# Performance work log

Measured on AMD Instinct MI355X. Metric: run time of the kernel, lower is better.

## Reference

```python
import jax, jax.numpy as jnp
import numpy as np

B, N, S = 2, 16384, 4096
IN_CH, OUT_CH = 256, 128

def setup_inputs() -> dict:
    key = jax.random.key(0)
    ks = jax.random.split(key, 8)
    down_xyzp = jax.random.normal(ks[0], (B, S, 4), dtype=jnp.float32)
    down_features = jax.random.normal(ks[1], (B, S, IN_CH), dtype=jnp.float32)
    ori_xyzp = jax.random.normal(ks[2], (B, N, 4), dtype=jnp.float32)
    ori_features = jax.random.normal(ks[3], (B, N, OUT_CH), dtype=jnp.float32)
    # Linear params (torch nn.Linear: y = x @ W.T + b); store as [in,out] for einsum
    W1 = jax.random.normal(ks[4], (IN_CH, OUT_CH), dtype=jnp.float32) / np.sqrt(IN_CH)
    b1 = jnp.zeros((OUT_CH,), dtype=jnp.float32)
    W2 = jax.random.normal(ks[5], (OUT_CH, OUT_CH), dtype=jnp.float32) / np.sqrt(OUT_CH)
    b2 = jnp.zeros((OUT_CH,), dtype=jnp.float32)
    return {"down_xyzp": down_xyzp, "down_features": down_features,
            "ori_xyzp": ori_xyzp, "ori_features": ori_features,
            "W1": W1, "b1": b1, "W2": W2, "b2": b2}

def reference(down_xyzp, down_features, ori_xyzp, ori_features, W1, b1, W2, b2):
    down_f = down_features @ W1 + b1          # [B,S,OUT]
    ori_f = ori_features @ W2 + b2            # [B,N,OUT]
    ori_xyz = ori_xyzp[..., :3]               # [B,N,3]
    down_xyz = down_xyzp[..., :3]             # [B,S,3]
    # squared pairwise dists [B,N,S] via expansion (avoids [B,N,S,3] intermediate)
    d2 = (jnp.sum(ori_xyz**2, -1)[:, :, None]
          + jnp.sum(down_xyz**2, -1)[:, None, :]
          - 2.0 * jnp.einsum('bnd,bsd->bns', ori_xyz, down_xyz))
    neg_top, idx = jax.lax.top_k(-d2, 3)      # 3 smallest dists, ascending
    dists = -neg_top                          # [B,N,3]
    dist_recip = 1.0 / (dists + 1e-8)
    weight = dist_recip / jnp.sum(dist_recip, axis=2, keepdims=True)  # [B,N,3]
    gathered = jax.vmap(lambda f, i: f[i])(down_f, idx)               # [B,N,3,OUT]
    interpolated = jnp.sum(gathered * weight[..., None], axis=2)      # [B,N,OUT]
    return ori_f + interpolated
```

## Files before the change

kernel.cpp:

```cpp
#include <hip/hip_runtime.h>
#include <hip/hip_bf16.h>
#include <float.h>

constexpr int B   = 2;
constexpr int N   = 16384;
constexpr int S   = 4096;
constexpr int INC = 256;
constexpr int OUTC = 128;

typedef short short4_t __attribute__((ext_vector_type(4)));
typedef short short8_t __attribute__((ext_vector_type(8)));
typedef float f32x4    __attribute__((ext_vector_type(4)));

__device__ __forceinline__ unsigned short f2bf(float f) {
    unsigned u = __builtin_bit_cast(unsigned, f);
    u += 0x7fffu + ((u >> 16) & 1u);
    return (unsigned short)(u >> 16);
}

template <int K, int ROWS>
__global__ __launch_bounds__(256) void k_mfma(const float* __restrict__ f,
                                              const float* __restrict__ W,
                                              const float* __restrict__ bias,
                                              float* __restrict__ outf) {
    constexpr int MF = ROWS / 16;
    constexpr int KS = K / 32;
    __shared__ __align__(16) short smem[K * 128];

    const int tid  = threadIdx.x;
    const int lane = tid & 63;
    const int wv   = tid >> 6;
    const int rowbase = blockIdx.x * ROWS;
    const int lo16 = lane & 15;
    const int hi8  = (lane >> 4) * 8;

    const float4* w4 = reinterpret_cast<const float4*>(W);
    for (int n = tid; n < K * 32; n += 256) {
        const float4 u = w4[n];
        short4_t s = { (short)f2bf(u.x), (short)f2bf(u.y),
                       (short)f2bf(u.z), (short)f2bf(u.w) };
        *reinterpret_cast<short4_t*>(&smem[n * 4]) = s;
    }
    __syncthreads();

    short8_t bf[KS][2];
    #pragma unroll
    for (int ks = 0; ks < KS; ++ks) {
        #pragma unroll
        for (int c = 0; c < 2; ++c) {
            const int col = wv * 32 + c * 16 + lo16;
            #pragma unroll
            for (int r = 0; r < 8; ++r)
                bf[ks][c][r] = smem[(ks * 32 + hi8 + r) * 128 + col];
        }
    }
    __syncthreads();

    const float4* a4 = reinterpret_cast<const float4*>(f + (size_t)rowbase * K);
    for (int n = tid; n < ROWS * K / 8; n += 256) {
        const int row   = n / (K / 8);
        const int k8    = (n % (K / 8)) * 8;
        const int base4 = (row * K + k8) >> 2;
        const float4 u = a4[base4];
        const float4 v = a4[base4 + 1];
        short8_t s = { (short)f2bf(u.x), (short)f2bf(u.y), (short)f2bf(u.z), (short)f2bf(u.w),
                       (short)f2bf(v.x), (short)f2bf(v.y), (short)f2bf(v.z), (short)f2bf(v.w) };
        const int idx = (row * K + k8) ^ ((row & 7) << 3);
        *reinterpret_cast<short8_t*>(&smem[idx]) = s;
    }
    __syncthreads();

    f32x4 acc[MF][2];
    #pragma unroll
    for (int m = 0; m < MF; ++m) {
        #pragma unroll
        for (int c = 0; c < 2; ++c) acc[m][c] = (f32x4){0.f, 0.f, 0.f, 0.f};
    }

    const int axor = (lane & 7) << 3;
    #pragma unroll
    for (int ks = 0; ks < KS; ++ks) {
        #pragma unroll
        for (int m = 0; m < MF; ++m) {
            const int aidx = ((m * 16 + lo16) * K + ks * 32 + hi8) ^ axor;
            const short8_t af = *reinterpret_cast<const short8_t*>(&smem[aidx]);
            acc[m][0] = __builtin_amdgcn_mfma_f32_16x16x32_bf16(af, bf[ks][0], acc[m][0], 0, 0, 0);
            acc[m][1] = __builtin_amdgcn_mfma_f32_16x16x32_bf16(af, bf[ks][1], acc[m][1], 0, 0, 0);
        }
    }

    #pragma unroll
    for (int c = 0; c < 2; ++c) {
        const int col = wv * 32 + c * 16 + lo16;
        const float bb = bias[col];
        #pragma unroll
        for (int m = 0; m < MF; ++m) {
            #pragma unroll
            for (int r = 0; r < 4; ++r) {
                const int row = rowbase + m * 16 + (lane >> 4) * 4 + r;
                outf[(size_t)row * 128 + col] = acc[m][c][r] + bb;
            }
        }
    }
}

#define INS3M(d0, d1, d2, i0, i1, i2, dd, ss)                               \
    {                                                                       \
        const bool c0 = (dd) < d0, c1 = (dd) < d1, c2 = (dd) < d2;          \
        i2 = c1 ? i1 : (c2 ? (ss) : i2);                                    \
        i1 = c0 ? i0 : (c1 ? (ss) : i1);                                    \
        i0 = c0 ? (ss) : i0;                                                \
        d2 = fminf(fmaxf((dd), d1), d2);                                    \
        d1 = fminf(fmaxf((dd), d0), d1);                                    \
        d0 = fminf(d0, (dd));                                               \
    }

#define INS3L(d0, d1, d2, i0, i1, i2, dd, ss)                               \
    {                                                                       \
        const bool c0 = ((dd) < d0) | (((dd) == d0) & ((ss) < i0));         \
        const bool c1 = ((dd) < d1) | (((dd) == d1) & ((ss) < i1));         \
        const bool c2 = ((dd) < d2) | (((dd) == d2) & ((ss) < i2));         \
        i2 = c1 ? i1 : (c2 ? (ss) : i2);                                    \
        i1 = c0 ? i0 : (c1 ? (ss) : i1);                                    \
        i0 = c0 ? (ss) : i0;                                                \
        d2 = c1 ? d1 : (c2 ? (dd) : d2);                                    \
        d1 = c0 ? d0 : (c1 ? (dd) : d1);                                    \
        d0 = c0 ? (dd) : d0;                                                \
    }

__global__ __launch_bounds__(256) void k_interp(const float4* __restrict__ dxyzp,
                                                const float4* __restrict__ oxyzp,
                                                const float*  __restrict__ downf,
                                                float*        __restrict__ out) {
    __shared__ float4 sx[16 * 65];
    __shared__ int    si[16 * 3];
    __shared__ float  sw[16 * 3];

    const int b     = blockIdx.x >> 10;
    const int qbase = (blockIdx.x & 1023) * 16;

    const int lane = threadIdx.x & 63;
    const int wave = threadIdx.x >> 6;
    const int sp   = lane & 15;
    const int qs   = lane >> 4;
    const int slot = wave * 4 + qs;

    const float4 o = oxyzp[(size_t)b * N + qbase + slot];
    const float sumo = __fadd_rn(__fadd_rn(__fmul_rn(o.x, o.x), __fmul_rn(o.y, o.y)),
                                 __fmul_rn(o.z, o.z));

    float a0 = FLT_MAX, a1 = FLT_MAX, a2 = FLT_MAX;
    int   ai0 = 0, ai1 = 0, ai2 = 0;

    const float4* dpb = dxyzp + (size_t)b * S;

    for (int c = 0; c < 4; ++c) {
        if (c > 0) __syncthreads();

        const float4* dpc = dpb + c * 1024;
        for (int j = threadIdx.x; j < 1024; j += 256) {
            float4 v = dpc[j];
            const float ss = __fadd_rn(__fadd_rn(__fmul_rn(v.x, v.x), __fmul_rn(v.y, v.y)),
                                       __fmul_rn(v.z, v.z));
            float4 w;
            w.x = v.x + v.x;
            w.y = v.y + v.y;
            w.z = v.z + v.z;
            w.w = ss;
            sx[(j >> 6) * 65 + (j & 63)] = w;
        }
        __syncthreads();

        const float4* base = &sx[sp * 65];
        const int g0 = c * 1024 + sp * 64;

        #pragma unroll 4
        for (int i = 0; i < 64; ++i) {
            const float4 q = base[i];
            const float dot2 = __fadd_rn(__fadd_rn(__fmul_rn(q.x, o.x), __fmul_rn(q.y, o.y)),
                                         __fmul_rn(q.z, o.z));
            const float dd = __fsub_rn(__fadd_rn(sumo, q.w), dot2);
            INS3M(a0, a1, a2, ai0, ai1, ai2, dd, g0 + i);
        }
    }

    #pragma unroll
    for (int m = 1; m <= 8; m <<= 1) {
        const float nd0 = __shfl_xor(a0, m, 64);
        const float nd1 = __shfl_xor(a1, m, 64);
        const float nd2 = __shfl_xor(a2, m, 64);
        const int   ni0 = __shfl_xor(ai0, m, 64);
        const int   ni1 = __shfl_xor(ai1, m, 64);
        const int   ni2 = __shfl_xor(ai2, m, 64);
        INS3L(a0, a1, a2, ai0, ai1, ai2, nd0, ni0);
        INS3L(a0, a1, a2, ai0, ai1, ai2, nd1, ni1);
        INS3L(a0, a1, a2, ai0, ai1, ai2, nd2, ni2);
    }

    if (sp == 0) {
        const float r0 = 1.0f / (a0 + 1e-8f);
        const float r1 = 1.0f / (a1 + 1e-8f);
        const float r2 = 1.0f / (a2 + 1e-8f);
        const float rs = __fadd_rn(__fadd_rn(r0, r1), r2);
        si[slot * 3 + 0] = ai0;
        si[slot * 3 + 1] = ai1;
        si[slot * 3 + 2] = ai2;
        sw[slot * 3 + 0] = r0 / rs;
        sw[slot * 3 + 1] = r1 / rs;
        sw[slot * 3 + 2] = r2 / rs;
    }
    __syncthreads();

    const int ch = threadIdx.x & 127;
    const int hf = threadIdx.x >> 7;
    const float* df = downf + (size_t)b * S * OUTC;
    float* ob = out + ((size_t)b * N + qbase) * OUTC;

    for (int pp = hf; pp < 16; pp += 2) {
        const int   j0 = si[pp * 3 + 0];
        const int   j1 = si[pp * 3 + 1];
        const int   j2 = si[pp * 3 + 2];
        const float w0 = sw[pp * 3 + 0];
        const float w1 = sw[pp * 3 + 1];
        const float w2 = sw[pp * 3 + 2];
        const float g = __fadd_rn(
            __fadd_rn(__fmul_rn(w0, df[(size_t)j0 * OUTC + ch]),
                      __fmul_rn(w1, df[(size_t)j1 * OUTC + ch])),
            __fmul_rn(w2, df[(size_t)j2 * OUTC + ch]));
        ob[(size_t)pp * OUTC + ch] += g;
    }
}


extern "C" void kernel_launch(void* const* d_in, const int* in_sizes, int n_in,
                              void* d_out, int out_size, void* d_ws, size_t ws_size,
                              hipStream_t stream) {
    const float* dxyzp = (const float*)d_in[0];
    const float* dfeat = (const float*)d_in[1];
    const float* oxyzp = (const float*)d_in[2];
    const float* ofeat = (const float*)d_in[3];
    const float* W1    = (const float*)d_in[4];
    const float* b1    = (const float*)d_in[5];
    const float* W2    = (const float*)d_in[6];
    const float* b2    = (const float*)d_in[7];

    float* out   = (float*)d_out;
    float* downf = (float*)d_ws;

    k_mfma<INC, 32><<<(B * S) / 32, 256, 0, stream>>>(dfeat, W1, b1, downf);
    k_mfma<OUTC, 64><<<(B * N) / 64, 256, 0, stream>>>(ofeat, W2, b2, out);
    k_interp<<<B * (N / 16), 256, 0, stream>>>(
        (const float4*)dxyzp, (const float4*)oxyzp, downf, out);
}
```

Before: 115.4 us.

## Fuse ori_features linear projection into the interpolation kernel

Removes the separate MFMA launch for ori_features @ W2 and computes each block's 16-row tile inside the interpolation kernel, converting W2 and the tile to bf16 in shared memory. The result plus bias is combined with the interpolated features and written once, so the out buffer is no longer written and then read-modify-written. The cost is that every one of the 2048 blocks reloads and converts the full 128x128 W2 matrix. It also adds LDS reuse and extra synchronization before the KNN search.

```diff
diff --git a/kernel.cpp b/kernel.cpp
--- a/kernel.cpp
+++ b/kernel.cpp
@@ -7,6 +7,8 @@
 constexpr int S   = 4096;
 constexpr int INC = 256;
 constexpr int OUTC = 128;
+
+constexpr size_t OFF_DOWNF = 0;
 
 typedef short short4_t __attribute__((ext_vector_type(4)));
 typedef short short8_t __attribute__((ext_vector_type(8)));
@@ -128,22 +130,77 @@
         d0 = c0 ? (dd) : d0;                                                \
     }
 
-__global__ __launch_bounds__(256) void k_interp(const float4* __restrict__ dxyzp,
-                                                const float4* __restrict__ oxyzp,
-                                                const float*  __restrict__ downf,
-                                                float*        __restrict__ out) {
-    __shared__ float4 sx[16 * 65];
-    __shared__ int    si[16 * 3];
-    __shared__ float  sw[16 * 3];
-
+__global__ __launch_bounds__(256) void k_fused(const float4* __restrict__ dxyzp,
+                                               const float4* __restrict__ oxyzp,
+                                               const float*  __restrict__ ofeat,
+                                               const float*  __restrict__ W2,
+                                               const float*  __restrict__ b2,
+                                               const float*  __restrict__ downf,
+                                               float*        __restrict__ out) {
+    __shared__ __align__(16) char lds[37248];
+    short*  sW = reinterpret_cast<short*>(lds);
+    short*  sA = reinterpret_cast<short*>(lds + 32768);
+    float4* sx = reinterpret_cast<float4*>(lds);
+    int*    si = reinterpret_cast<int*>(lds + 36864);
+    float*  sw = reinterpret_cast<float*>(lds + 37056);
+
+    const int tid  = threadIdx.x;
+    const int lane = tid & 63;
+    const int wv   = tid >> 6;
     const int b     = blockIdx.x >> 10;
     const int qbase = (blockIdx.x & 1023) * 16;
-
-    const int lane = threadIdx.x & 63;
-    const int wave = threadIdx.x >> 6;
+    const int lo16 = lane & 15;
+    const int hi8  = (lane >> 4) * 8;
+
+    const float4* w4 = reinterpret_cast<const float4*>(W2);
+    for (int n = tid; n < 128 * 32; n += 256) {
+        const float4 u = w4[n];
+        short4_t s = { (short)f2bf(u.x), (short)f2bf(u.y),
+                       (short)f2bf(u.z), (short)f2bf(u.w) };
+        *reinterpret_cast<short4_t*>(&sW[n * 4]) = s;
+    }
+    {
+        const float4* a4 = reinterpret_cast<const float4*>(
+            ofeat + (size_t)(b * N + qbase) * 128);
+        const int n    = tid;
+        const int row  = n >> 4;
+        const int k8   = (n & 15) * 8;
+        const int base4 = (row * 128 + k8) >> 2;
+        const float4 u = a4[base4];
+        const float4 v = a4[base4 + 1];
+        short8_t s = { (short)f2bf(u.x), (short)f2bf(u.y), (short)f2bf(u.z), (short)f2bf(u.w),
+                       (short)f2bf(v.x), (short)f2bf(v.y), (short)f2bf(v.z), (short)f2bf(v.w) };
+        const int idx = (row * 128 + k8) ^ ((row & 7) << 3);
+        *reinterpret_cast<short8_t*>(&sA[idx]) = s;
+    }
+    __syncthreads();
+
+    short8_t bfr[4][2];
+    #pragma unroll
+    for (int ks = 0; ks < 4; ++ks) {
+        #pragma unroll
+        for (int c = 0; c < 2; ++c) {
+            const int col = wv * 32 + c * 16 + lo16;
+            #pragma unroll
+            for (int r = 0; r < 8; ++r)
+                bfr[ks][c][r] = sW[(ks * 32 + hi8 + r) * 128 + col];
+        }
+    }
+
+    f32x4 acc[2] = { (f32x4){0.f,0.f,0.f,0.f}, (f32x4){0.f,0.f,0.f,0.f} };
+    const int axor = (lane & 7) << 3;
+    #pragma unroll
+    for (int ks = 0; ks < 4; ++ks) {
+        const int aidx = (lo16 * 128 + ks * 32 + hi8) ^ axor;
+        const short8_t af = *reinterpret_cast<const short8_t*>(&sA[aidx]);
+        acc[0] = __builtin_amdgcn_mfma_f32_16x16x32_bf16(af, bfr[ks][0], acc[0], 0, 0, 0);
+        acc[1] = __builtin_amdgcn_mfma_f32_16x16x32_bf16(af, bfr[ks][1], acc[1], 0, 0, 0);
+    }
+    __syncthreads();
+
     const int sp   = lane & 15;
     const int qs   = lane >> 4;
-    const int slot = wave * 4 + qs;
+    const int slot = wv * 4 + qs;
 
     const float4 o = oxyzp[(size_t)b * N + qbase + slot];
     const float sumo = __fadd_rn(__fadd_rn(__fmul_rn(o.x, o.x), __fmul_rn(o.y, o.y)),
@@ -156,9 +213,8 @@
 
     for (int c = 0; c < 4; ++c) {
         if (c > 0) __syncthreads();
-
         const float4* dpc = dpb + c * 1024;
-        for (int j = threadIdx.x; j < 1024; j += 256) {
+        for (int j = tid; j < 1024; j += 256) {
             float4 v = dpc[j];
             const float ss = __fadd_rn(__fadd_rn(__fmul_rn(v.x, v.x), __fmul_rn(v.y, v.y)),
                                        __fmul_rn(v.z, v.z));
@@ -211,23 +267,28 @@
     }
     __syncthreads();
 
-    const int ch = threadIdx.x & 127;
-    const int hf = threadIdx.x >> 7;
     const float* df = downf + (size_t)b * S * OUTC;
-    float* ob = out + ((size_t)b * N + qbase) * OUTC;
-
-    for (int pp = hf; pp < 16; pp += 2) {
-        const int   j0 = si[pp * 3 + 0];
-        const int   j1 = si[pp * 3 + 1];
-        const int   j2 = si[pp * 3 + 2];
-        const float w0 = sw[pp * 3 + 0];
-        const float w1 = sw[pp * 3 + 1];
-        const float w2 = sw[pp * 3 + 2];
-        const float g = __fadd_rn(
-            __fadd_rn(__fmul_rn(w0, df[(size_t)j0 * OUTC + ch]),
-                      __fmul_rn(w1, df[(size_t)j1 * OUTC + ch])),
-            __fmul_rn(w2, df[(size_t)j2 * OUTC + ch]));
-        ob[(size_t)pp * OUTC + ch] += g;
+    float* ob = out + (size_t)(b * N + qbase) * OUTC;
+
+    #pragma unroll
+    for (int c = 0; c < 2; ++c) {
+        const int col = wv * 32 + c * 16 + lo16;
+        const float bb = b2[col];
+        #pragma unroll
+        for (int r = 0; r < 4; ++r) {
+            const int row16 = (lane >> 4) * 4 + r;
+            const int   j0 = si[row16 * 3 + 0];
+            const int   j1 = si[row16 * 3 + 1];
+            const int   j2 = si[row16 * 3 + 2];
+            const float w0 = sw[row16 * 3 + 0];
+            const float w1 = sw[row16 * 3 + 1];
+            const float w2 = sw[row16 * 3 + 2];
+            const float g = __fadd_rn(
+                __fadd_rn(__fmul_rn(w0, df[(size_t)j0 * OUTC + col]),
+                          __fmul_rn(w1, df[(size_t)j1 * OUTC + col])),
+                __fmul_rn(w2, df[(size_t)j2 * OUTC + col]));
+            ob[(size_t)row16 * OUTC + col] = (acc[c][r] + bb) + g;
+        }
     }
 }
 
@@ -245,10 +306,10 @@
     const float* b2    = (const float*)d_in[7];
 
     float* out   = (float*)d_out;
-    float* downf = (float*)d_ws;
+    float* downf = (float*)((char*)d_ws + OFF_DOWNF);
 
     k_mfma<INC, 32><<<(B * S) / 32, 256, 0, stream>>>(dfeat, W1, b1, downf);
-    k_mfma<OUTC, 64><<<(B * N) / 64, 256, 0, stream>>>(ofeat, W2, b2, out);
-    k_interp<<<B * (N / 16), 256, 0, stream>>>(
-        (const float4*)dxyzp, (const float4*)oxyzp, downf, out);
+
+    k_fused<<<B * (N / 16), 256, 0, stream>>>(
+        (const float4*)dxyzp, (const float4*)oxyzp, ofeat, W2, b2, downf, out);
 }
```

Result: faster. 108.8 us (-5.7%).
